# Performance work log

Hardware: AMD Instinct MI355X
Metric: run time of the kernel (lower is better)

The kernel has to match this reference:

```python
import jax, jax.numpy as jnp
import numpy as np

B, T, C, H = 8, 1024, 1536, 12
D = C // H  # head_size = 128
EPS = 1e-5


def layer_norm(x, g, b):
    m = jnp.mean(x, axis=-1, keepdims=True)
    v = jnp.var(x, axis=-1, keepdims=True)
    return (x - m) / jnp.sqrt(v + EPS) * g + b


def batch_norm_T(x, g, b):
    # BatchNorm1d(block_size) on (B, T, C): channels are the T axis;
    # training-mode batch statistics over (B, C), biased variance.
    m = jnp.mean(x, axis=(0, 2), keepdims=True)
    v = jnp.var(x, axis=(0, 2), keepdims=True)
    return (x - m) / jnp.sqrt(v + EPS) * g[None, :, None] + b[None, :, None]


def setup_inputs() -> dict:
    key = jax.random.key(0)
    ks = jax.random.split(key, 12)
    s = 0.02
    inp = {
        "x": jax.random.normal(ks[0], (B, T, C), dtype=jnp.float32),
        # per-head q/k/v projections stacked: (H, C, D)
        "wq": jax.random.normal(ks[1], (H, C, D), dtype=jnp.float32) * s,
        "wk": jax.random.normal(ks[2], (H, C, D), dtype=jnp.float32) * s,
        "wv": jax.random.normal(ks[3], (H, C, D), dtype=jnp.float32) * s,
        "wo": jax.random.normal(ks[4], (C, C), dtype=jnp.float32) * s,
        "bo": jnp.zeros((C,), dtype=jnp.float32),
        "ln1_g": jnp.ones((C,), dtype=jnp.float32),
        "ln1_b": jnp.zeros((C,), dtype=jnp.float32),
        "ln2_g": jnp.ones((C,), dtype=jnp.float32),
        "ln2_b": jnp.zeros((C,), dtype=jnp.float32),
        "w1": jax.random.normal(ks[5], (C, 4 * C), dtype=jnp.float32) * s,
        "b1": jnp.zeros((4 * C,), dtype=jnp.float32),
        "w2": jax.random.normal(ks[6], (4 * C, C), dtype=jnp.float32) * s,
        "b2": jnp.zeros((C,), dtype=jnp.float32),
        "bn1_g": jnp.ones((T,), dtype=jnp.float32),
        "bn1_b": jnp.zeros((T,), dtype=jnp.float32),
        "bn2_g": jnp.ones((T,), dtype=jnp.float32),
        "bn2_b": jnp.zeros((T,), dtype=jnp.float32),
    }
    return inp


def reference(x, wq, wk, wv, wo, bo, ln1_g, ln1_b, ln2_g, ln2_b,
              w1, b1, w2, b2, bn1_g, bn1_b, bn2_g, bn2_b):
    # --- multi-head causal self-attention (pre-LN) ---
    h = layer_norm(x, ln1_g, ln1_b)                       # (B,T,C)
    q = jnp.einsum('btc,hcd->bhtd', h, wq)
    k = jnp.einsum('btc,hcd->bhtd', h, wk)
    v = jnp.einsum('btc,hcd->bhtd', h, wv)
    scores = jnp.einsum('bhtd,bhsd->bhts', q, k) * (D ** -0.5)
    causal = jnp.tril(jnp.ones((T, T), dtype=bool))
    scores = jnp.where(causal, scores, -jnp.inf)
    attn = jax.nn.softmax(scores, axis=-1)                # dropout = identity (eval)
    o = jnp.einsum('bhts,bhsd->bthd', attn, v).reshape(B, T, C)
    sa = o @ wo + bo
    x = x + sa
    x = batch_norm_T(x, bn1_g, bn1_b)
    # --- feed-forward ---
    h2 = layer_norm(x, ln2_g, ln2_b)
    ff = jax.nn.relu(h2 @ w1 + b1) @ w2 + b2
    x = batch_norm_T(x + ff, bn2_g, bn2_b)
    return x
```

## Files before the change

### kernel.cpp

```cpp
#include <hip/hip_runtime.h>
#include <hip/hip_bf16.h>

constexpr int BATCH = 8;
constexpr int SEQ   = 1024;
constexpr int CH    = 1536;
constexpr int NH    = 12;
constexpr int HD    = 128;
constexpr int FFDIM = 6144;
constexpr int NROWS = BATCH * SEQ;
constexpr int QKVLD = 3 * CH;
constexpr float EPS = 1e-5f;

typedef unsigned short ushort;
typedef __attribute__((ext_vector_type(8))) ushort us8;
typedef __attribute__((ext_vector_type(8))) __bf16 bf16x8;
typedef __attribute__((ext_vector_type(4))) float f32x4;

__device__ __forceinline__ float b2f(ushort u) {
  return __uint_as_float(((unsigned)u) << 16);
}
__device__ __forceinline__ ushort f2b(float f) {
  __hip_bfloat16 h = __float2bfloat16(f);
  return *reinterpret_cast<ushort*>(&h);
}

__device__ __forceinline__ void g2l16(const ushort* g, ushort* l) {
  __builtin_amdgcn_global_load_lds(
      (const __attribute__((address_space(1))) void*)g,
      (__attribute__((address_space(3))) void*)l, 16, 0, 0);
}

__device__ __forceinline__ float block_sum(float v, float* red) {
#pragma unroll
  for (int o = 32; o > 0; o >>= 1) v += __shfl_down(v, o, 64);
  const int w = threadIdx.x >> 6;
  if ((threadIdx.x & 63) == 0) red[w] = v;
  __syncthreads();
  const float r = red[0] + red[1] + red[2] + red[3];
  __syncthreads();
  return r;
}

__global__ __launch_bounds__(256) void ln_bf16(const float* __restrict__ x,
                                               const float* __restrict__ g,
                                               const float* __restrict__ b,
                                               ushort* __restrict__ out) {
  __shared__ float row[CH];
  __shared__ float red[4];
  const size_t base = (size_t)blockIdx.x * CH;
  float s = 0.f;
  for (int c = threadIdx.x; c < CH; c += 256) {
    const float v = x[base + c];
    row[c] = v;
    s += v;
  }
  const float mean = block_sum(s, red) * (1.0f / CH);
  float s2 = 0.f;
  for (int c = threadIdx.x; c < CH; c += 256) {
    const float d = row[c] - mean;
    s2 += d * d;
  }
  const float var = block_sum(s2, red) * (1.0f / CH);
  const float rstd = rsqrtf(var + EPS);
  for (int c = threadIdx.x; c < CH; c += 256)
    out[base + c] = f2b((row[c] - mean) * rstd * g[c] + b[c]);
}

__global__ __launch_bounds__(256) void transpose_cast(const float* __restrict__ src,
                                                      ushort* __restrict__ dst,
                                                      int R, int Cc, int ldd,
                                                      long srcZ, long dstZ) {
  __shared__ float tile[32][33];
  src += (size_t)blockIdx.z * srcZ;
  dst += (size_t)blockIdx.z * dstZ;
  const int c0 = blockIdx.x * 32, r0 = blockIdx.y * 32;
  const int tx = threadIdx.x & 31, ty = threadIdx.x >> 5;
#pragma unroll
  for (int i = ty; i < 32; i += 8)
    tile[i][tx] = src[(size_t)(r0 + i) * Cc + c0 + tx];
  __syncthreads();
#pragma unroll
  for (int i = ty; i < 32; i += 8)
    dst[(size_t)(c0 + i) * ldd + r0 + tx] = f2b(tile[tx][i]);
}

__global__ __launch_bounds__(256) void transpose_v(const ushort* __restrict__ src,
                                                   ushort* __restrict__ dst) {
  __shared__ ushort tile[32][33];
  const int bh = blockIdx.z;
  const int b = bh / NH, h = bh % NH;
  const ushort* s = src + (size_t)b * SEQ * QKVLD + (size_t)h * HD;
  ushort* d = dst + (size_t)bh * HD * SEQ;
  const int t0 = blockIdx.x * 32, d0 = blockIdx.y * 32;
  const int tx = threadIdx.x & 31, ty = threadIdx.x >> 5;
#pragma unroll
  for (int i = ty; i < 32; i += 8)
    tile[i][tx] = s[(size_t)(t0 + i) * QKVLD + d0 + tx];
  __syncthreads();
#pragma unroll
  for (int i = ty; i < 32; i += 8)
    d[(size_t)(d0 + i) * SEQ + t0 + tx] = tile[tx][i];
}

constexpr int BT = 128;
constexpr int BK = 32;

template <int RELU, int BIAS, int RES, int OUTBF, int ATOMIC = 0>
__global__ __launch_bounds__(256) void gemm_bf16(
    const ushort* __restrict__ A, int lda,
    const ushort* __restrict__ Bt, int ldb,
    void* __restrict__ Cm, int ldc,
    const float* __restrict__ bias,
    const float* __restrict__ res, int ldr,
    int K) {
  __shared__ ushort As[2][BT * BK];
  __shared__ ushort Bs[2][BT * BK];
  const int tid = threadIdx.x;
  const int lane = tid & 63;
  const int wv = tid >> 6;
  const int m0 = blockIdx.y * BT;
  const int n0 = blockIdx.x * BT;
  if (ATOMIC) {
    const size_t kz = (size_t)blockIdx.z * K;
    A += kz;
    Bt += kz;
  }
  const int srow = wv * 32 + (lane >> 2);
  const int sx = (srow >> 1) & 3;
  const int schunk = ((lane & 3) ^ sx) * 8;
  const ushort* gA0 = A + (size_t)(m0 + srow) * lda + schunk;
  const ushort* gA1 = gA0 + (size_t)16 * lda;
  const ushort* gB0 = Bt + (size_t)(n0 + srow) * ldb + schunk;
  const ushort* gB1 = gB0 + (size_t)16 * ldb;
  const int lofs = (wv * 32) * BK;
  const int wm = (wv >> 1) * 64, wn = (wv & 1) * 64;
  const int fr = lane & 15;
  const int quad = lane >> 4;
  const int koff = (quad ^ ((fr >> 1) & 3)) * 8;

  f32x4 acc[4][4] = {{}};
  g2l16(gA0, &As[0][lofs]);
  g2l16(gA1, &As[0][lofs + 16 * BK]);
  g2l16(gB0, &Bs[0][lofs]);
  g2l16(gB1, &Bs[0][lofs + 16 * BK]);
  __syncthreads();
  int buf = 0;
  for (int k0 = 0; k0 < K; k0 += BK) {
    const int nk = k0 + BK;
    if (nk < K) {
      g2l16(gA0 + nk, &As[buf ^ 1][lofs]);
      g2l16(gA1 + nk, &As[buf ^ 1][lofs + 16 * BK]);
      g2l16(gB0 + nk, &Bs[buf ^ 1][lofs]);
      g2l16(gB1 + nk, &Bs[buf ^ 1][lofs + 16 * BK]);
    }
    bf16x8 af[4], bf[4];
#pragma unroll
    for (int mi = 0; mi < 4; ++mi)
      af[mi] = *(const bf16x8*)&As[buf][(wm + mi * 16 + fr) * BK + koff];
#pragma unroll
    for (int ni = 0; ni < 4; ++ni)
      bf[ni] = *(const bf16x8*)&Bs[buf][(wn + ni * 16 + fr) * BK + koff];
#pragma unroll
    for (int mi = 0; mi < 4; ++mi)
#pragma unroll
      for (int ni = 0; ni < 4; ++ni)
        acc[mi][ni] = __builtin_amdgcn_mfma_f32_16x16x32_bf16(af[mi], bf[ni], acc[mi][ni], 0, 0, 0);
    __syncthreads();
    buf ^= 1;
  }
#pragma unroll
  for (int ni = 0; ni < 4; ++ni) {
    const int col = n0 + wn + ni * 16 + fr;
    const float bs = (BIAS && (!ATOMIC || blockIdx.z == 0)) ? bias[col] : 0.f;
#pragma unroll
    for (int mi = 0; mi < 4; ++mi) {
      const int rowb = m0 + wm + mi * 16 + quad * 4;
#pragma unroll
      for (int r = 0; r < 4; ++r) {
        float v = acc[mi][ni][r] + bs;
        if (RELU) v = fmaxf(v, 0.f);
        const size_t idx = (size_t)(rowb + r) * ldc + col;
        if (RES) v += res[(size_t)(rowb + r) * ldr + col];
        if (ATOMIC)      atomicAdd((float*)Cm + idx, v);
        else if (OUTBF)  ((ushort*)Cm)[idx] = f2b(v);
        else             ((float*)Cm)[idx] = v;
      }
    }
  }
}

constexpr int FQT = 64;
constexpr int VLD = 72;

__global__ __launch_bounds__(256) void flash_attn_mfma(
    const ushort* __restrict__ q, const ushort* __restrict__ k,
    const ushort* __restrict__ vt, ushort* __restrict__ o,
    int ld, int ldo) {
  __shared__ ushort Ks[2][64 * 128];
  __shared__ ushort Vs[2][128 * 64];
  __shared__ ushort Ps[4][16][VLD];
  const int tid = threadIdx.x;
  const int lane = tid & 63;
  const int w = tid >> 6;
  const int fr = lane & 15;
  const int quad = lane >> 4;
  const int qt = blockIdx.x;
  const int b = blockIdx.y / NH;
  const int h = blockIdx.y % NH;
  const size_t base = (size_t)b * SEQ * ld + (size_t)h * HD;
  const ushort* vtb = vt + (size_t)(b * NH + h) * HD * SEQ;
  const int q0 = qt * FQT;
  const int qrow = q0 + w * 16;
  const float scale = 0.08838834764831845f;

  const ushort* gk[4];
  const ushort* gv[4];
#pragma unroll
  for (int t = 0; t < 4; ++t) {
    const int jr = w * 16 + t * 4 + (lane >> 4);
    const int kc = (lane & 15) ^ (jr & 7);
    gk[t] = k + base + (size_t)jr * ld + kc * 8;
    const int dr = w * 32 + t * 8 + (lane >> 3);
    const int vc = (lane & 7) ^ (dr & 7);
    gv[t] = vtb + (size_t)dr * SEQ + vc * 8;
  }

  bf16x8 aq[4];
  {
    const ushort* qp = q + base + (size_t)(qrow + fr) * ld + quad * 8;
#pragma unroll
    for (int ks = 0; ks < 4; ++ks) aq[ks] = *(const bf16x8*)(qp + ks * 32);
  }

  float m_i[4], l_i[4];
  f32x4 oacc[8];
#pragma unroll
  for (int i = 0; i < 4; ++i) { m_i[i] = -3.0e38f; l_i[i] = 0.f; }
#pragma unroll
  for (int n8 = 0; n8 < 8; ++n8) oacc[n8] = (f32x4){0.f, 0.f, 0.f, 0.f};

#pragma unroll
  for (int t = 0; t < 4; ++t) {
    g2l16(gk[t], &Ks[0][w * 2048 + t * 512]);
    g2l16(gv[t], &Vs[0][w * 2048 + t * 512]);
  }
  __syncthreads();

  int cur = 0;
  for (int jt = 0; jt <= qt; ++jt) {
    const int j0 = jt * FQT;
    if (jt < qt) {
      const size_t ko = (size_t)(jt + 1) * FQT * ld;
      const int vo = (jt + 1) * FQT;
      ushort* kd = (cur ? &Ks[0][0] : &Ks[1][0]) + w * 2048;
      ushort* vd = (cur ? &Vs[0][0] : &Vs[1][0]) + w * 2048;
#pragma unroll
      for (int t = 0; t < 4; ++t) {
        g2l16(gk[t] + ko, kd + t * 512);
        g2l16(gv[t] + vo, vd + t * 512);
      }
    }
    const ushort* Kc = cur ? &Ks[1][0] : &Ks[0][0];
    const ushort* Vc = cur ? &Vs[1][0] : &Vs[0][0];

    f32x4 sacc[4];
#pragma unroll
    for (int ni = 0; ni < 4; ++ni) sacc[ni] = (f32x4){0.f, 0.f, 0.f, 0.f};
#pragma unroll
    for (int ks = 0; ks < 4; ++ks) {
#pragma unroll
      for (int ni = 0; ni < 4; ++ni) {
        const int j = ni * 16 + fr;
        const int s = (ks * 4 + quad) ^ (fr & 7);
        const bf16x8 kf = *(const bf16x8*)&Kc[j * 128 + s * 8];
        sacc[ni] = __builtin_amdgcn_mfma_f32_16x16x32_bf16(aq[ks], kf, sacc[ni], 0, 0, 0);
      }
    }
    const bool diag = (jt == qt);
    float alpha[4];
#pragma unroll
    for (int i = 0; i < 4; ++i) {
      const int qg = qrow + quad * 4 + i;
      float pv[4];
      float vmax = -3.0e38f;
#pragma unroll
      for (int ni = 0; ni < 4; ++ni) {
        float sv = sacc[ni][i] * scale;
        if (diag && (j0 + ni * 16 + fr > qg)) sv = -3.0e38f;
        pv[ni] = sv;
        vmax = fmaxf(vmax, sv);
      }
#pragma unroll
      for (int mm = 8; mm >= 1; mm >>= 1) vmax = fmaxf(vmax, __shfl_xor(vmax, mm, 64));
      const float m_new = fmaxf(m_i[i], vmax);
      alpha[i] = __expf(m_i[i] - m_new);
      m_i[i] = m_new;
      float rsum = 0.f;
#pragma unroll
      for (int ni = 0; ni < 4; ++ni) {
        const float pe = __expf(pv[ni] - m_new);
        Ps[w][quad * 4 + i][ni * 16 + fr] = f2b(pe);
        rsum += pe;
      }
#pragma unroll
      for (int mm = 8; mm >= 1; mm >>= 1) rsum += __shfl_xor(rsum, mm, 64);
      l_i[i] = l_i[i] * alpha[i] + rsum;
#pragma unroll
      for (int n8 = 0; n8 < 8; ++n8) oacc[n8][i] *= alpha[i];
    }
#pragma unroll
    for (int js = 0; js < 2; ++js) {
      const bf16x8 pf = *(const bf16x8*)&Ps[w][fr][js * 32 + quad * 8];
#pragma unroll
      for (int n8 = 0; n8 < 8; ++n8) {
        const int d = n8 * 16 + fr;
        const int s = (js * 4 + quad) ^ (fr & 7);
        const bf16x8 vf = *(const bf16x8*)&Vc[d * 64 + s * 8];
        oacc[n8] = __builtin_amdgcn_mfma_f32_16x16x32_bf16(pf, vf, oacc[n8], 0, 0, 0);
      }
    }
    __syncthreads();
    cur ^= 1;
  }
#pragma unroll
  for (int i = 0; i < 4; ++i) {
    const float inv = 1.0f / l_i[i];
    ushort* op = o + ((size_t)b * SEQ + qrow + quad * 4 + i) * ldo + (size_t)h * HD;
#pragma unroll
    for (int n8 = 0; n8 < 8; ++n8) op[n8 * 16 + fr] = f2b(oacc[n8][i] * inv);
  }
}

__global__ __launch_bounds__(256) void bn_stats(const float* __restrict__ x,
                                                float* __restrict__ mean,
                                                float* __restrict__ rstd) {
  __shared__ float red[4];
  const int t = blockIdx.x;
  float s = 0.f;
  for (int bb = 0; bb < BATCH; ++bb) {
    const float* p = x + ((size_t)bb * SEQ + t) * CH;
    for (int c = threadIdx.x; c < CH; c += 256) s += p[c];
  }
  const float m = block_sum(s, red) * (1.0f / (BATCH * CH));
  float s2 = 0.f;
  for (int bb = 0; bb < BATCH; ++bb) {
    const float* p = x + ((size_t)bb * SEQ + t) * CH;
    for (int c = threadIdx.x; c < CH; c += 256) {
      const float d = p[c] - m;
      s2 += d * d;
    }
  }
  const float var = block_sum(s2, red) * (1.0f / (BATCH * CH));
  if (threadIdx.x == 0) {
    mean[t] = m;
    rstd[t] = rsqrtf(var + EPS);
  }
}

__global__ __launch_bounds__(256) void bn_apply(const float* __restrict__ x,
                                                float* __restrict__ out,
                                                const float* __restrict__ mean,
                                                const float* __restrict__ rstd,
                                                const float* __restrict__ g,
                                                const float* __restrict__ bb) {
  const size_t i = (size_t)blockIdx.x * 256 + threadIdx.x;
  const int t = (int)((i / CH) % SEQ);
  out[i] = (x[i] - mean[t]) * rstd[t] * g[t] + bb[t];
}

extern "C" void kernel_launch(void* const* d_in, const int* in_sizes, int n_in,
                              void* d_out, int out_size, void* d_ws, size_t ws_size,
                              hipStream_t stream) {
  const float* x    = (const float*)d_in[0];
  const float* wq   = (const float*)d_in[1];
  const float* wk   = (const float*)d_in[2];
  const float* wv   = (const float*)d_in[3];
  const float* wo   = (const float*)d_in[4];
  const float* bo   = (const float*)d_in[5];
  const float* ln1g = (const float*)d_in[6];
  const float* ln1b = (const float*)d_in[7];
  const float* ln2g = (const float*)d_in[8];
  const float* ln2b = (const float*)d_in[9];
  const float* w1   = (const float*)d_in[10];
  const float* b1   = (const float*)d_in[11];
  const float* w2   = (const float*)d_in[12];
  const float* b2   = (const float*)d_in[13];
  const float* bn1g = (const float*)d_in[14];
  const float* bn1b = (const float*)d_in[15];
  const float* bn2g = (const float*)d_in[16];
  const float* bn2b = (const float*)d_in[17];
  float* out = (float*)d_out;

  ushort* wsu = (ushort*)d_ws;
  const size_t NCs   = (size_t)NROWS * CH;
  ushort* R0    = wsu;
  ushort* QKV   = wsu + NCs;
  ushort* wqkvT = wsu + NCs + (size_t)NROWS * QKVLD;
  ushort* woT   = wqkvT + (size_t)QKVLD * CH;
  float*  meanp = (float*)(woT + (size_t)CH * CH);
  float*  rstdp = meanp + SEQ;
  ushort* w1T   = QKV;
  ushort* w2T   = QKV + (size_t)FFDIM * CH;
  ushort* FF1   = QKV + 2 * (size_t)FFDIM * CH;

  const dim3 blk(256);

  transpose_cast<<<dim3(HD / 32, CH / 32, NH), blk, 0, stream>>>(
      wq, wqkvT, CH, HD, CH, (long)CH * HD, (long)HD * CH);
  transpose_cast<<<dim3(HD / 32, CH / 32, NH), blk, 0, stream>>>(
      wk, wqkvT + (size_t)CH * CH, CH, HD, CH, (long)CH * HD, (long)HD * CH);
  transpose_cast<<<dim3(HD / 32, CH / 32, NH), blk, 0, stream>>>(
      wv, wqkvT + 2 * (size_t)CH * CH, CH, HD, CH, (long)CH * HD, (long)HD * CH);
  transpose_cast<<<dim3(CH / 32, CH / 32, 1), blk, 0, stream>>>(
      wo, woT, CH, CH, CH, 0, 0);

  ln_bf16<<<NROWS, blk, 0, stream>>>(x, ln1g, ln1b, R0);

  gemm_bf16<0, 0, 0, 1><<<dim3(QKVLD / BT, NROWS / BT), blk, 0, stream>>>(
      R0, CH, wqkvT, CH, QKV, QKVLD, nullptr, nullptr, 0, CH);

  transpose_v<<<dim3(SEQ / 32, HD / 32, BATCH * NH), blk, 0, stream>>>(
      QKV + 2 * CH, R0);

  flash_attn_mfma<<<dim3(SEQ / FQT, BATCH * NH), blk, 0, stream>>>(
      QKV, QKV + CH, R0, QKV, QKVLD, QKVLD);

  gemm_bf16<0, 1, 1, 0><<<dim3(CH / BT, NROWS / BT), blk, 0, stream>>>(
      QKV, QKVLD, woT, CH, out, CH, bo, x, CH, CH);

  transpose_cast<<<dim3(FFDIM / 32, CH / 32, 1), blk, 0, stream>>>(
      w1, w1T, CH, FFDIM, CH, 0, 0);
  transpose_cast<<<dim3(CH / 32, FFDIM / 32, 1), blk, 0, stream>>>(
      w2, w2T, FFDIM, CH, FFDIM, 0, 0);

  bn_stats<<<SEQ, blk, 0, stream>>>(out, meanp, rstdp);
  bn_apply<<<(NROWS * CH) / 256, blk, 0, stream>>>(out, out, meanp, rstdp, bn1g, bn1b);

  ln_bf16<<<NROWS, blk, 0, stream>>>(out, ln2g, ln2b, R0);

  constexpr int FFC = 4096;
  for (int c = 0; c < NROWS / FFC; ++c) {
    const size_t r0 = (size_t)c * FFC;
    gemm_bf16<1, 1, 0, 1><<<dim3(FFDIM / BT, FFC / BT), blk, 0, stream>>>(
        R0 + r0 * CH, CH, w1T, CH, FF1, FFDIM, b1, nullptr, 0, CH);
    gemm_bf16<0, 1, 0, 0, 1><<<dim3(CH / BT, FFC / BT, 2), blk, 0, stream>>>(
        FF1, FFDIM, w2T, FFDIM, out + r0 * CH, CH, b2, nullptr, 0, FFDIM / 2);
  }

  bn_stats<<<SEQ, blk, 0, stream>>>(out, meanp, rstdp);
  bn_apply<<<(NROWS * CH) / 256, blk, 0, stream>>>(out, out, meanp, rstdp, bn2g, bn2b);
}
```

Measured before the change: 1.182 ms.

## Add 256x256-tile GEMM with 4-stage LDS pipeline for QKV and FF1

```diff
diff --git a/kernel.cpp b/kernel.cpp
--- a/kernel.cpp
+++ b/kernel.cpp
@@ -100,6 +100,109 @@
 #pragma unroll
   for (int i = ty; i < 32; i += 8)
     d[(size_t)(d0 + i) * SEQ + t0 + tx] = tile[tx][i];
+}
+
+constexpr int GBK = 32;
+
+#define G256_STAGE(T, B)                                     \
+  g2l16(pA0 + (size_t)(T) * GBK, &As[B][lq]);                \
+  g2l16(pA1 + (size_t)(T) * GBK, &As[B][lq + 16 * GBK]);     \
+  g2l16(pB0 + (size_t)(T) * GBK, &Bs[B][lq]);                \
+  g2l16(pB1 + (size_t)(T) * GBK, &Bs[B][lq + 16 * GBK]);
+
+#define G256_WAITBAR(T)                                                               \
+  if ((T) + 3 < NT)      asm volatile("s_waitcnt vmcnt(8) lgkmcnt(0)" ::: "memory");  \
+  else if ((T) + 2 < NT) asm volatile("s_waitcnt vmcnt(4) lgkmcnt(0)" ::: "memory");  \
+  else                   asm volatile("s_waitcnt vmcnt(0) lgkmcnt(0)" ::: "memory");  \
+  __builtin_amdgcn_s_barrier();
+
+#define G256_WINDOW(T, B)                                                             \
+  {                                                                                   \
+    bf16x8 bfm[4], afm[4];                                                            \
+    _Pragma("unroll") for (int n = 0; n < 4; ++n)                                     \
+      bfm[n] = *(const bf16x8*)&Bs[B][(wn + n * 16 + fr) * GBK + koff];               \
+    _Pragma("unroll") for (int m = 0; m < 4; ++m)                                     \
+      afm[m] = *(const bf16x8*)&As[B][(wm + m * 16 + fr) * GBK + koff];               \
+    if ((T) + 3 < NT) { G256_STAGE((T) + 3, ((B) + 3) & 3) }                          \
+    __builtin_amdgcn_s_setprio(1);                                                    \
+    _Pragma("unroll") for (int m = 0; m < 4; ++m)                                     \
+      _Pragma("unroll") for (int n = 0; n < 4; ++n)                                   \
+        acc[m][n] = __builtin_amdgcn_mfma_f32_16x16x32_bf16(afm[m], bfm[n],           \
+                                                            acc[m][n], 0, 0, 0);      \
+    __builtin_amdgcn_s_setprio(0);                                                    \
+    _Pragma("unroll") for (int m = 0; m < 4; ++m)                                     \
+      afm[m] = *(const bf16x8*)&As[B][(wm + (m + 4) * 16 + fr) * GBK + koff];         \
+    __builtin_amdgcn_s_setprio(1);                                                    \
+    _Pragma("unroll") for (int m = 0; m < 4; ++m)                                     \
+      _Pragma("unroll") for (int n = 0; n < 4; ++n)                                   \
+        acc[m + 4][n] = __builtin_amdgcn_mfma_f32_16x16x32_bf16(afm[m], bfm[n],       \
+                                                                acc[m + 4][n], 0, 0, 0); \
+    __builtin_amdgcn_s_setprio(0);                                                    \
+    G256_WAITBAR(T)                                                                   \
+  }
+
+template <int RELU, int BIAS, int OUTBF>
+__global__ __launch_bounds__(512, 2) void gemm256(
+    const ushort* __restrict__ A, int lda,
+    const ushort* __restrict__ Bt, int ldb,
+    void* __restrict__ Cm, int ldc,
+    const float* __restrict__ bias,
+    int K, int nbx) {
+  __shared__ ushort As[4][256 * GBK];
+  __shared__ ushort Bs[4][256 * GBK];
+  const int tid = threadIdx.x;
+  const int lane = tid & 63;
+  const int wv = tid >> 6;
+  int bid = blockIdx.x;
+  const int cpx = gridDim.x >> 3;
+  bid = (bid & 7) * cpx + (bid >> 3);
+  const int m0 = (bid / nbx) * 256;
+  const int n0 = (bid % nbx) * 256;
+  const int srow = lane >> 2;
+  const int sgc = ((lane & 3) ^ ((lane >> 3) & 3)) * 8;
+  const ushort* pA0 = A + (size_t)(m0 + wv * 32 + srow) * lda + sgc;
+  const ushort* pA1 = pA0 + (size_t)16 * lda;
+  const ushort* pB0 = Bt + (size_t)(n0 + wv * 32 + srow) * ldb + sgc;
+  const ushort* pB1 = pB0 + (size_t)16 * ldb;
+  const int lq = (wv * 32) * GBK;
+  const int wm = (wv >> 2) * 128;
+  const int wn = (wv & 3) * 64;
+  const int fr = lane & 15;
+  const int quad = lane >> 4;
+  const int koff = (quad ^ ((fr >> 1) & 3)) * 8;
+  const int NT = K >> 5;
+
+  f32x4 acc[8][4] = {{}};
+  G256_STAGE(0, 0)
+  G256_STAGE(1, 1)
+  G256_STAGE(2, 2)
+  asm volatile("s_waitcnt vmcnt(8)" ::: "memory");
+  __builtin_amdgcn_s_barrier();
+
+  for (int t = 0; t < NT; t += 4) {
+    G256_WINDOW(t + 0, 0)
+    G256_WINDOW(t + 1, 1)
+    G256_WINDOW(t + 2, 2)
+    G256_WINDOW(t + 3, 3)
+  }
+
+#pragma unroll
+  for (int n = 0; n < 4; ++n) {
+    const int col = n0 + wn + n * 16 + fr;
+    const float bs = BIAS ? bias[col] : 0.f;
+#pragma unroll
+    for (int m = 0; m < 8; ++m) {
+      const int rowb = m0 + wm + m * 16 + quad * 4;
+#pragma unroll
+      for (int r = 0; r < 4; ++r) {
+        float v = acc[m][n][r] + bs;
+        if (RELU) v = fmaxf(v, 0.f);
+        const size_t idx = (size_t)(rowb + r) * ldc + col;
+        if (OUTBF) ((ushort*)Cm)[idx] = f2b(v);
+        else       ((float*)Cm)[idx] = v;
+      }
+    }
+  }
 }
 
 constexpr int BT = 128;
@@ -416,8 +519,8 @@
 
   ln_bf16<<<NROWS, blk, 0, stream>>>(x, ln1g, ln1b, R0);
 
-  gemm_bf16<0, 0, 0, 1><<<dim3(QKVLD / BT, NROWS / BT), blk, 0, stream>>>(
-      R0, CH, wqkvT, CH, QKV, QKVLD, nullptr, nullptr, 0, CH);
+  gemm256<0, 0, 1><<<dim3((NROWS / 256) * (QKVLD / 256)), dim3(512), 0, stream>>>(
+      R0, CH, wqkvT, CH, QKV, QKVLD, nullptr, CH, QKVLD / 256);
 
   transpose_v<<<dim3(SEQ / 32, HD / 32, BATCH * NH), blk, 0, stream>>>(
       QKV + 2 * CH, R0);
@@ -441,8 +544,8 @@
   constexpr int FFC = 4096;
   for (int c = 0; c < NROWS / FFC; ++c) {
     const size_t r0 = (size_t)c * FFC;
-    gemm_bf16<1, 1, 0, 1><<<dim3(FFDIM / BT, FFC / BT), blk, 0, stream>>>(
-        R0 + r0 * CH, CH, w1T, CH, FF1, FFDIM, b1, nullptr, 0, CH);
+    gemm256<1, 1, 1><<<dim3((FFC / 256) * (FFDIM / 256)), dim3(512), 0, stream>>>(
+        R0 + r0 * CH, CH, w1T, CH, FF1, FFDIM, b1, CH, FFDIM / 256);
     gemm_bf16<0, 1, 0, 0, 1><<<dim3(CH / BT, FFC / BT, 2), blk, 0, stream>>>(
         FF1, FFDIM, w2T, FFDIM, out + r0 * CH, CH, b2, nullptr, 0, FFDIM / 2);
   }
```

Result: no change. 1.203 ms (+1.7%).

## Add 256x256-tile 512-thread bf16 GEMM for QKV and FFN1 projections

Applied to the files above, without the earlier changes.

```diff
diff --git a/kernel.cpp b/kernel.cpp
--- a/kernel.cpp
+++ b/kernel.cpp
@@ -100,6 +100,119 @@
 #pragma unroll
   for (int i = ty; i < 32; i += 8)
     d[(size_t)(d0 + i) * SEQ + t0 + tx] = tile[tx][i];
+}
+
+constexpr int PBK = 64;
+
+#define P_STAGE_A(T, H)                                                        \
+  g2l16(pA[H][0] + (size_t)(T) * PBK, &As[(T) & 1][((H) * 128 + wv * 16) * PBK]); \
+  g2l16(pA[H][1] + (size_t)(T) * PBK, &As[(T) & 1][((H) * 128 + wv * 16 + 8) * PBK]);
+#define P_STAGE_B(T, H)                                                        \
+  g2l16(pB[H][0] + (size_t)(T) * PBK, &Bs[(T) & 1][((H) * 128 + wv * 16) * PBK]); \
+  g2l16(pB[H][1] + (size_t)(T) * PBK, &Bs[(T) & 1][((H) * 128 + wv * 16 + 8) * PBK]);
+
+#define P_RD_B(KOFF)                                            \
+  _Pragma("unroll") for (int n = 0; n < 4; ++n)                 \
+      bfm[n] = *(const bf16x8*)&Bsb[(wn + n * 16 + fr) * PBK + (KOFF)];
+#define P_RD_A(MB, KOFF)                                        \
+  _Pragma("unroll") for (int m = 0; m < 4; ++m)                 \
+      afm[m] = *(const bf16x8*)&Asb[(wm + ((MB) + m) * 16 + fr) * PBK + (KOFF)];
+
+#define P_MFMA(MB)                                                             \
+  __builtin_amdgcn_s_setprio(1);                                               \
+  _Pragma("unroll") for (int m = 0; m < 4; ++m)                                \
+      _Pragma("unroll") for (int n = 0; n < 4; ++n)                            \
+          acc[(MB) + m][n] = __builtin_amdgcn_mfma_f32_16x16x32_bf16(          \
+              afm[m], bfm[n], acc[(MB) + m][n], 0, 0, 0);                      \
+  __builtin_amdgcn_s_setprio(0);
+
+#define P_BAR __builtin_amdgcn_s_barrier();
+
+template <int RELU, int BIAS, int OUTBF>
+__global__ __launch_bounds__(512, 2) void gemm256(
+    const ushort* __restrict__ A, int lda,
+    const ushort* __restrict__ Bt, int ldb,
+    void* __restrict__ Cm, int ldc,
+    const float* __restrict__ bias,
+    int K, int nbx) {
+  __shared__ ushort As[2][256 * PBK];
+  __shared__ ushort Bs[2][256 * PBK];
+  const int tid = threadIdx.x;
+  const int lane = tid & 63;
+  const int wv = tid >> 6;
+  int bid = blockIdx.x;
+  const int cpx = gridDim.x >> 3;
+  bid = (bid & 7) * cpx + (bid >> 3);
+  const int m0 = (bid / nbx) * 256;
+  const int n0 = (bid % nbx) * 256;
+  const int sr = lane >> 3;
+  const int sc = ((lane & 7) ^ sr) * 8;
+  const ushort* pA[2][2];
+  const ushort* pB[2][2];
+#pragma unroll
+  for (int h = 0; h < 2; ++h)
+#pragma unroll
+    for (int i = 0; i < 2; ++i) {
+      const int r = h * 128 + wv * 16 + i * 8 + sr;
+      pA[h][i] = A + (size_t)(m0 + r) * lda + sc;
+      pB[h][i] = Bt + (size_t)(n0 + r) * ldb + sc;
+    }
+  const int wm = (wv >> 2) * 128;
+  const int wn = (wv & 3) * 64;
+  const int fr = lane & 15;
+  const int quad = lane >> 4;
+  const int k0off = (quad ^ (fr & 7)) * 8;
+  const int k1off = k0off ^ 32;
+  const int NT = K / PBK;
+
+  f32x4 acc[8][4] = {{}};
+  P_STAGE_A(0, 0) P_STAGE_A(0, 1) P_STAGE_B(0, 0) P_STAGE_B(0, 1)
+  P_STAGE_A(1, 0)
+  asm volatile("s_waitcnt vmcnt(2)" ::: "memory");
+  P_BAR
+
+  for (int t = 0; t < NT; ++t) {
+    const ushort* Asb = As[t & 1];
+    const ushort* Bsb = Bs[t & 1];
+    const bool st = (t + 1 < NT);
+    bf16x8 afm[4], bfm[4];
+    P_RD_B(k0off) P_RD_A(0, k0off)
+    if (st) { P_STAGE_A(t + 1, 1) }
+    P_BAR P_MFMA(0) P_BAR
+    P_RD_A(4, k0off)
+    if (st) { P_STAGE_B(t + 1, 0) }
+    P_BAR P_MFMA(4) P_BAR
+    P_RD_B(k1off) P_RD_A(0, k1off)
+    if (st) { P_STAGE_B(t + 1, 1) }
+    P_BAR P_MFMA(0) P_BAR
+    P_RD_A(4, k1off)
+    P_BAR P_MFMA(4) P_BAR
+    if (t + 2 < NT) {
+      P_STAGE_A(t + 2, 0)
+      asm volatile("s_waitcnt vmcnt(2)" ::: "memory");
+    } else if (t + 1 < NT) {
+      asm volatile("s_waitcnt vmcnt(0)" ::: "memory");
+    }
+    if (t + 1 < NT) P_BAR
+  }
+
+#pragma unroll
+  for (int n = 0; n < 4; ++n) {
+    const int col = n0 + wn + n * 16 + fr;
+    const float bs = BIAS ? bias[col] : 0.f;
+#pragma unroll
+    for (int m = 0; m < 8; ++m) {
+      const int rowb = m0 + wm + m * 16 + quad * 4;
+#pragma unroll
+      for (int r = 0; r < 4; ++r) {
+        float v = acc[m][n][r] + bs;
+        if (RELU) v = fmaxf(v, 0.f);
+        const size_t idx = (size_t)(rowb + r) * ldc + col;
+        if (OUTBF) ((ushort*)Cm)[idx] = f2b(v);
+        else       ((float*)Cm)[idx] = v;
+      }
+    }
+  }
 }
 
 constexpr int BT = 128;
@@ -416,8 +529,8 @@
 
   ln_bf16<<<NROWS, blk, 0, stream>>>(x, ln1g, ln1b, R0);
 
-  gemm_bf16<0, 0, 0, 1><<<dim3(QKVLD / BT, NROWS / BT), blk, 0, stream>>>(
-      R0, CH, wqkvT, CH, QKV, QKVLD, nullptr, nullptr, 0, CH);
+  gemm256<0, 0, 1><<<dim3((NROWS / 256) * (QKVLD / 256)), dim3(512), 0, stream>>>(
+      R0, CH, wqkvT, CH, QKV, QKVLD, nullptr, CH, QKVLD / 256);
 
   transpose_v<<<dim3(SEQ / 32, HD / 32, BATCH * NH), blk, 0, stream>>>(
       QKV + 2 * CH, R0);
@@ -441,8 +554,8 @@
   constexpr int FFC = 4096;
   for (int c = 0; c < NROWS / FFC; ++c) {
     const size_t r0 = (size_t)c * FFC;
-    gemm_bf16<1, 1, 0, 1><<<dim3(FFDIM / BT, FFC / BT), blk, 0, stream>>>(
-        R0 + r0 * CH, CH, w1T, CH, FF1, FFDIM, b1, nullptr, 0, CH);
+    gemm256<1, 1, 1><<<dim3((FFC / 256) * (FFDIM / 256)), dim3(512), 0, stream>>>(
+        R0 + r0 * CH, CH, w1T, CH, FF1, FFDIM, b1, CH, FFDIM / 256);
     gemm_bf16<0, 1, 0, 0, 1><<<dim3(CH / BT, FFC / BT, 2), blk, 0, stream>>>(
         FF1, FFDIM, w2T, FFDIM, out + r0 * CH, CH, b2, nullptr, 0, FFDIM / 2);
   }
```

Measured after the change: 1.259 ms. +6.5%, slower.
